# Performance work log

Hardware: AMD Instinct MI355X
Metric: run time of the kernel (lower is better)

Reference implementation:

```python
import jax, jax.numpy as jnp
import numpy as np

DAMPING = 0.3
RES_SIZE = 2048
N_FEATURE = 8
N_READOUT = 8
T = 4096

def setup_inputs() -> dict:
    key = jax.random.key(0)
    k1, k2, k3, k4 = jax.random.split(key, 4)
    inp = jax.random.normal(k1, (T, N_FEATURE), dtype=jnp.float32)
    Win = jax.random.normal(k2, (1 + N_FEATURE, RES_SIZE), dtype=jnp.float32) * 0.1
    W = jax.random.normal(k3, (RES_SIZE, RES_SIZE), dtype=jnp.float32) * (1.25 / jnp.sqrt(RES_SIZE))
    Wout = jax.random.normal(k4, (1 + N_FEATURE + RES_SIZE, N_READOUT), dtype=jnp.float32) * 0.02
    return {"inp": inp, "Win": Win, "W": W, "Wout": Wout}

def reference(inp, Win, W, Wout):
    # ESN.predict: leaky-integrator reservoir recurrence + linear readout.
    d = jnp.asarray(DAMPING, dtype=inp.dtype)
    win_bias, win_u = Win[0], Win[1:]                      # [R], [F,R]
    wout_bias = Wout[0]                                    # [O]
    wout_u = Wout[1:1 + N_FEATURE]                         # [F,O]
    wout_x = Wout[1 + N_FEATURE:]                          # [R,O]
    # precompute input drive for all timesteps: [T,R]
    drive = win_bias + inp @ win_u

    def step(x, args):
        dr_t, u_t = args
        x_new = (1 - d) * x + d * jnp.tanh(dr_t + x @ W)   # [R]
        y = wout_bias + u_t @ wout_u + x_new @ wout_x      # [O]
        return x_new, y

    x0 = jnp.zeros((RES_SIZE,), dtype=inp.dtype)
    _, Y = jax.lax.scan(step, x0, (drive, inp))
    return Y  # [T, n_readout]
```

## Files before the change

### kernel.cpp

```cpp
#include <hip/hip_runtime.h>
#include <math.h>

#define T_STEPS 4096
#define RES     2048
#define NF      8
#define NR      8
#define K_WG    512
#define WTHR    64
#define NTHR    256
#define SENTINEL 2.0f
#define VALID_MASK 0x7fffffffu
#define VALID_LIM  0x3f800000u
#define DBLK 32

typedef unsigned long long u64;
typedef unsigned int       u32;

__global__ void k_drive(const float* __restrict__ inp, const float* __restrict__ Win,
                        float* __restrict__ drive) {
    int idx = blockIdx.x * blockDim.x + threadIdx.x;
    int t = idx >> 11;
    int j = idx & (RES - 1);
    float d = Win[j];
#pragma unroll
    for (int f = 0; f < NF; ++f)
        d += inp[t * NF + f] * Win[(1 + f) * RES + j];
    drive[idx] = d;
}

__global__ void k_init(float* __restrict__ X) {
    int tid = threadIdx.x + blockIdx.x * blockDim.x;
    int stride = blockDim.x * gridDim.x;
    const int total = (T_STEPS + 1) * RES;
    for (int i = tid; i < total; i += stride)
        X[i] = (i < RES) ? 0.f : SENTINEL;
}

__global__ __launch_bounds__(WTHR, 1) void k_recur(
        const float* __restrict__ W, const float* __restrict__ drive,
        float* __restrict__ X) {
    const int lane = threadIdx.x & 63;
    const int g    = blockIdx.x;
    const int c0   = g * 4;

    float4 Wr[32];
#pragma unroll
    for (int i = 0; i < 16; ++i) {
        size_t r0 = (size_t)(2 * lane + 128 * i);
        Wr[2 * i]     = *reinterpret_cast<const float4*>(&W[r0 * RES + c0]);
        Wr[2 * i + 1] = *reinterpret_cast<const float4*>(&W[(r0 + 1) * RES + c0]);
    }
#pragma unroll
    for (int i = 0; i < 32; ++i)
        asm volatile("" : "+v"(Wr[i].x), "+v"(Wr[i].y), "+v"(Wr[i].z), "+v"(Wr[i].w));

    float xprev = 0.f;

    auto drv_addr = [&](int tb) {
        return reinterpret_cast<const u64*>(
                   &drive[(size_t)(tb + (lane >> 1)) * RES + c0 + (lane & 1) * 2]);
    };
    u64 dcur = *drv_addr(0);
    u64 dnxt = *drv_addr(DBLK);

    u64 xv[16];
    {
        const u64* r0 = reinterpret_cast<const u64*>(X);
#pragma unroll
        for (int i = 0; i < 16; ++i)
            xv[i] = __hip_atomic_load(&r0[i * 64 + lane],
                                      __ATOMIC_RELAXED, __HIP_MEMORY_SCOPE_AGENT);
    }

    for (int t = 0; t < T_STEPS; ++t) {
        const u64* xrow64 = reinterpret_cast<const u64*>(X + (size_t)t * RES);

        int spins = 0;
        for (;;) {
            u32 m = 0;
#pragma unroll
            for (int i = 0; i < 16; ++i) {
                u32 lo = (u32)(xv[i])       & VALID_MASK;
                u32 hi = (u32)(xv[i] >> 32) & VALID_MASK;
                u32 mx = lo > hi ? lo : hi;
                m = m > mx ? m : mx;
            }
            if (__all(m < VALID_LIM)) break;
            if (++spins > 64) __builtin_amdgcn_s_sleep(1);
#pragma unroll
            for (int i = 0; i < 16; ++i)
                xv[i] = __hip_atomic_load(&xrow64[i * 64 + lane],
                                          __ATOMIC_RELAXED, __HIP_MEMORY_SCOPE_AGENT);
        }

        const int s = t & (DBLK - 1);
        float dr;
        {
            float lo = __uint_as_float((u32)dcur);
            float hi = __uint_as_float((u32)(dcur >> 32));
            int   src = 2 * s + ((lane & 3) >> 1);
            float v0 = __shfl(lo, src, 64);
            float v1 = __shfl(hi, src, 64);
            dr = (lane & 1) ? v1 : v0;
        }
        if (s == DBLK - 1 && t + 1 < T_STEPS) {
            dcur = dnxt;
            int tb2 = t + 1 + DBLK;
            if (tb2 < T_STEPS) dnxt = *drv_addr(tb2);
        }

        float a0 = 0.f, a1 = 0.f, a2 = 0.f, a3 = 0.f;
#pragma unroll
        for (int i = 0; i < 16; ++i) {
            float xlo = __uint_as_float((u32)xv[i]);
            float xhi = __uint_as_float((u32)(xv[i] >> 32));
            float4 wl = Wr[2 * i];
            float4 wh = Wr[2 * i + 1];
            a0 = fmaf(xlo, wl.x, a0); a0 = fmaf(xhi, wh.x, a0);
            a1 = fmaf(xlo, wl.y, a1); a1 = fmaf(xhi, wh.y, a1);
            a2 = fmaf(xlo, wl.z, a2); a2 = fmaf(xhi, wh.z, a2);
            a3 = fmaf(xlo, wl.w, a3); a3 = fmaf(xhi, wh.w, a3);
        }

        {
            const u64* nrow64 = reinterpret_cast<const u64*>(
                                    X + (size_t)(t + 1) * RES);
#pragma unroll
            for (int i = 0; i < 16; ++i)
                xv[i] = __hip_atomic_load(&nrow64[i * 64 + lane],
                                          __ATOMIC_RELAXED, __HIP_MEMORY_SCOPE_AGENT);
        }

        const bool b0 = (lane & 1) != 0;
        const bool b1 = (lane & 2) != 0;
        float u  = b0 ? a1 : a0;
        float v  = b0 ? a0 : a1;
        u += __shfl_xor(v, 1, 64);
        float w2 = b0 ? a3 : a2;
        float z2 = b0 ? a2 : a3;
        w2 += __shfl_xor(z2, 1, 64);
        float p  = b1 ? w2 : u;
        float q  = b1 ? u : w2;
        p += __shfl_xor(q, 2, 64);
        p += __shfl_xor(p, 4, 64);
        p += __shfl_xor(p, 8, 64);
        p += __shfl_xor(p, 16, 64);
        p += __shfl_xor(p, 32, 64);

        if (lane < 4) {
            float ss = dr + p;
            float e  = __expf(2.0f * ss);
            float th = 1.0f - 2.0f * __builtin_amdgcn_rcpf(e + 1.0f);
            float xn = 0.7f * xprev + 0.3f * th;
            __hip_atomic_store(&X[(size_t)(t + 1) * RES + c0 + lane], xn,
                               __ATOMIC_RELAXED, __HIP_MEMORY_SCOPE_AGENT);
            xprev = xn;
        }
    }
}

__global__ void k_readout(const float* __restrict__ inp, const float* __restrict__ Wout,
                          const float* __restrict__ X, float* __restrict__ Y) {
    int t   = blockIdx.x;
    int tid = threadIdx.x;
    int r   = tid & (NR - 1);
    int gph = tid >> 3;
    const float* x = X + (size_t)(t + 1) * RES;
    float p = 0.f;
#pragma unroll 4
    for (int m = 0; m < RES / 32; ++m) {
        int j = gph * (RES / 32) + m;
        p += x[j] * Wout[(size_t)(1 + NF + j) * NR + r];
    }
    __shared__ float red[NTHR];
    red[tid] = p;
    __syncthreads();
    for (int s = NTHR / 2; s >= NR; s >>= 1) {
        if (tid < s) red[tid] += red[tid + s];
        __syncthreads();
    }
    if (tid < NR) {
        float y = Wout[tid];
#pragma unroll
        for (int f = 0; f < NF; ++f)
            y += inp[t * NF + f] * Wout[(1 + f) * NR + tid];
        Y[t * NR + tid] = y + red[tid];
    }
}

extern "C" void kernel_launch(void* const* d_in, const int* in_sizes, int n_in,
                              void* d_out, int out_size, void* d_ws, size_t ws_size,
                              hipStream_t stream) {
    const float* inp  = (const float*)d_in[0];
    const float* Win  = (const float*)d_in[1];
    const float* W    = (const float*)d_in[2];
    const float* Wout = (const float*)d_in[3];
    float* Y = (float*)d_out;

    float* drive = (float*)d_ws;
    float* X     = drive + (size_t)T_STEPS * RES;

    k_init<<<2048, NTHR, 0, stream>>>(X);
    k_drive<<<(T_STEPS * RES) / NTHR, NTHR, 0, stream>>>(inp, Win, drive);
    k_recur<<<K_WG, WTHR, 0, stream>>>(W, drive, X);
    k_readout<<<T_STEPS, NTHR, 0, stream>>>(inp, Wout, X, Y);
}
```

Baseline: 6.398 ms.

## Double-buffer spin polling and use DPP adds for cross-lane reduction

```diff
diff --git a/kernel.cpp b/kernel.cpp
--- a/kernel.cpp
+++ b/kernel.cpp
@@ -16,6 +16,14 @@
 typedef unsigned long long u64;
 typedef unsigned int       u32;
 
+#define DPP_ADD(x, ctrl)                                                      \
+    x += __int_as_float(__builtin_amdgcn_mov_dpp(__float_as_int(x),           \
+                                                 (ctrl), 0xf, 0xf, true))
+#define DPP_XOR1 0xB1
+#define DPP_XOR2 0x4E
+#define DPP_ROR4 0x124
+#define DPP_ROR8 0x128
+
 __global__ void k_drive(const float* __restrict__ inp, const float* __restrict__ Win,
                         float* __restrict__ drive) {
     int idx = blockIdx.x * blockDim.x + threadIdx.x;
@@ -63,34 +71,61 @@
     u64 dcur = *drv_addr(0);
     u64 dnxt = *drv_addr(DBLK);
 
-    u64 xv[16];
+    u64 xp[16], xq[16];
     {
         const u64* r0 = reinterpret_cast<const u64*>(X);
 #pragma unroll
         for (int i = 0; i < 16; ++i)
-            xv[i] = __hip_atomic_load(&r0[i * 64 + lane],
+            xp[i] = __hip_atomic_load(&r0[i * 64 + lane],
                                       __ATOMIC_RELAXED, __HIP_MEMORY_SCOPE_AGENT);
     }
 
     for (int t = 0; t < T_STEPS; ++t) {
         const u64* xrow64 = reinterpret_cast<const u64*>(X + (size_t)t * RES);
 
+#pragma unroll
+        for (int i = 0; i < 16; ++i)
+            xq[i] = __hip_atomic_load(&xrow64[i * 64 + lane],
+                                      __ATOMIC_RELAXED, __HIP_MEMORY_SCOPE_AGENT);
+
         int spins = 0;
+        bool useQ = false;
         for (;;) {
-            u32 m = 0;
-#pragma unroll
-            for (int i = 0; i < 16; ++i) {
-                u32 lo = (u32)(xv[i])       & VALID_MASK;
-                u32 hi = (u32)(xv[i] >> 32) & VALID_MASK;
-                u32 mx = lo > hi ? lo : hi;
-                m = m > mx ? m : mx;
+            {
+                u32 m = 0;
+#pragma unroll
+                for (int i = 0; i < 16; ++i) {
+                    u32 lo = (u32)(xp[i])       & VALID_MASK;
+                    u32 hi = (u32)(xp[i] >> 32) & VALID_MASK;
+                    u32 mx = lo > hi ? lo : hi;
+                    m = m > mx ? m : mx;
+                }
+                if (__all(m < VALID_LIM)) break;
             }
-            if (__all(m < VALID_LIM)) break;
-            if (++spins > 64) __builtin_amdgcn_s_sleep(1);
 #pragma unroll
             for (int i = 0; i < 16; ++i)
-                xv[i] = __hip_atomic_load(&xrow64[i * 64 + lane],
+                xp[i] = __hip_atomic_load(&xrow64[i * 64 + lane],
                                           __ATOMIC_RELAXED, __HIP_MEMORY_SCOPE_AGENT);
+            {
+                u32 m = 0;
+#pragma unroll
+                for (int i = 0; i < 16; ++i) {
+                    u32 lo = (u32)(xq[i])       & VALID_MASK;
+                    u32 hi = (u32)(xq[i] >> 32) & VALID_MASK;
+                    u32 mx = lo > hi ? lo : hi;
+                    m = m > mx ? m : mx;
+                }
+                if (__all(m < VALID_LIM)) { useQ = true; break; }
+            }
+#pragma unroll
+            for (int i = 0; i < 16; ++i)
+                xq[i] = __hip_atomic_load(&xrow64[i * 64 + lane],
+                                          __ATOMIC_RELAXED, __HIP_MEMORY_SCOPE_AGENT);
+            if (++spins > 32) __builtin_amdgcn_s_sleep(1);
+        }
+        if (useQ) {
+#pragma unroll
+            for (int i = 0; i < 16; ++i) xp[i] = xq[i];
         }
 
         const int s = t & (DBLK - 1);
@@ -112,8 +147,8 @@
         float a0 = 0.f, a1 = 0.f, a2 = 0.f, a3 = 0.f;
 #pragma unroll
         for (int i = 0; i < 16; ++i) {
-            float xlo = __uint_as_float((u32)xv[i]);
-            float xhi = __uint_as_float((u32)(xv[i] >> 32));
+            float xlo = __uint_as_float((u32)xp[i]);
+            float xhi = __uint_as_float((u32)(xp[i] >> 32));
             float4 wl = Wr[2 * i];
             float4 wh = Wr[2 * i + 1];
             a0 = fmaf(xlo, wl.x, a0); a0 = fmaf(xhi, wh.x, a0);
@@ -122,30 +157,20 @@
             a3 = fmaf(xlo, wl.w, a3); a3 = fmaf(xhi, wh.w, a3);
         }
 
-        {
-            const u64* nrow64 = reinterpret_cast<const u64*>(
-                                    X + (size_t)(t + 1) * RES);
-#pragma unroll
-            for (int i = 0; i < 16; ++i)
-                xv[i] = __hip_atomic_load(&nrow64[i * 64 + lane],
-                                          __ATOMIC_RELAXED, __HIP_MEMORY_SCOPE_AGENT);
-        }
-
-        const bool b0 = (lane & 1) != 0;
-        const bool b1 = (lane & 2) != 0;
-        float u  = b0 ? a1 : a0;
-        float v  = b0 ? a0 : a1;
-        u += __shfl_xor(v, 1, 64);
-        float w2 = b0 ? a3 : a2;
-        float z2 = b0 ? a2 : a3;
-        w2 += __shfl_xor(z2, 1, 64);
-        float p  = b1 ? w2 : u;
-        float q  = b1 ? u : w2;
-        p += __shfl_xor(q, 2, 64);
-        p += __shfl_xor(p, 4, 64);
-        p += __shfl_xor(p, 8, 64);
-        p += __shfl_xor(p, 16, 64);
-        p += __shfl_xor(p, 32, 64);
+        DPP_ADD(a0, DPP_XOR1); DPP_ADD(a1, DPP_XOR1);
+        DPP_ADD(a2, DPP_XOR1); DPP_ADD(a3, DPP_XOR1);
+        DPP_ADD(a0, DPP_XOR2); DPP_ADD(a1, DPP_XOR2);
+        DPP_ADD(a2, DPP_XOR2); DPP_ADD(a3, DPP_XOR2);
+        DPP_ADD(a0, DPP_ROR4); DPP_ADD(a1, DPP_ROR4);
+        DPP_ADD(a2, DPP_ROR4); DPP_ADD(a3, DPP_ROR4);
+        DPP_ADD(a0, DPP_ROR8); DPP_ADD(a1, DPP_ROR8);
+        DPP_ADD(a2, DPP_ROR8); DPP_ADD(a3, DPP_ROR8);
+        float ac = (lane & 1) ? ((lane & 2) ? a3 : a1)
+                              : ((lane & 2) ? a2 : a0);
+        float t1 = __shfl(ac, (lane + 16) & 63, 64);
+        float t2 = __shfl(ac, (lane + 32) & 63, 64);
+        float t3 = __shfl(ac, (lane + 48) & 63, 64);
+        float p  = ac + t1 + t2 + t3;
 
         if (lane < 4) {
             float ss = dr + p;
@@ -155,6 +180,15 @@
             __hip_atomic_store(&X[(size_t)(t + 1) * RES + c0 + lane], xn,
                                __ATOMIC_RELAXED, __HIP_MEMORY_SCOPE_AGENT);
             xprev = xn;
+        }
+
+        {
+            const u64* nrow64 = reinterpret_cast<const u64*>(
+                                    X + (size_t)(t + 1) * RES);
+#pragma unroll
+            for (int i = 0; i < 16; ++i)
+                xp[i] = __hip_atomic_load(&nrow64[i * 64 + lane],
+                                          __ATOMIC_RELAXED, __HIP_MEMORY_SCOPE_AGENT);
         }
     }
 }
```

After: 17.71 ms. 177% more time.
